# Kernel tuning notes

Hardware: AMD Instinct MI355X
Metric: run time of the kernel (lower is better)

Reference implementation:

```python
import jax, jax.numpy as jnp
import numpy as np

N = 100000   # nodes
E = 1600000  # edges
IN = 128     # input_dim
H = 64       # hidden_dim
OUT = 2      # output_dim
G = 64       # number of graphs in the batch


def setup_inputs() -> dict:
    key = jax.random.key(0)
    ks = jax.random.split(key, 12)
    x = jax.random.normal(ks[0], (N, IN), dtype=jnp.float32)
    edge_index = jax.random.randint(ks[1], (2, E), 0, N, dtype=jnp.int64)
    batch = jnp.sort(jax.random.randint(ks[2], (N,), 0, G, dtype=jnp.int64))
    s = 0.05
    return {
        "x": x,
        "edge_index": edge_index,
        "batch": batch,
        "W1": jax.random.normal(ks[3], (IN, H), dtype=jnp.float32) * s,
        "b1": jnp.zeros((H,), dtype=jnp.float32),
        "W2": jax.random.normal(ks[4], (H, H), dtype=jnp.float32) * s,
        "b2": jnp.zeros((H,), dtype=jnp.float32),
        "W3": jax.random.normal(ks[5], (H, H), dtype=jnp.float32) * s,
        "b3": jnp.zeros((H,), dtype=jnp.float32),
        "Wm1": jax.random.normal(ks[6], (H, H), dtype=jnp.float32) * s,
        "bm1": jnp.zeros((H,), dtype=jnp.float32),
        "Wm2": jax.random.normal(ks[7], (H, OUT), dtype=jnpp.float32) * s if False else jax.random.normal(ks[7], (H, OUT), dtype=jnp.float32) * s,
        "bm2": jnp.zeros((OUT,), dtype=jnp.float32),
    }


def _gcn_conv(x, W, b, src, dst, norm, n_nodes):
    # PyG GCNConv: h = x @ W; message = norm * h[src]; scatter-add at dst; + bias
    h = x @ W                                  # [N, H]
    msg = h[src] * norm[:, None]               # [E+N, H] gather + scale
    out = jax.ops.segment_sum(msg, dst, num_segments=n_nodes)
    return out + b


def reference(x, edge_index, batch, W1, b1, W2, b2, W3, b3, Wm1, bm1, Wm2, bm2):
    n = x.shape[0]
    # add self-loops (PyG GCNConv default add_self_loops=True)
    loop = jnp.arange(n, dtype=edge_index.dtype)
    src = jnp.concatenate([edge_index[0], loop])
    dst = jnp.concatenate([edge_index[1], loop])
    # symmetric normalization deg^-1/2 (deg over target nodes, incl. self-loops)
    deg = jax.ops.segment_sum(jnp.ones_like(dst, dtype=x.dtype), dst, num_segments=n)
    dinv = jnp.where(deg > 0, jax.lax.rsqrt(deg), 0.0)
    norm = dinv[src] * dinv[dst]               # [E+N]

    h = jax.nn.relu(_gcn_conv(x, W1, b1, src, dst, norm, n))   # dropout: eval -> identity
    h = jax.nn.relu(_gcn_conv(h, W2, b2, src, dst, norm, n))
    h = jax.nn.relu(_gcn_conv(h, W3, b3, src, dst, norm, n))

    # global_mean_pool over batch ids
    sums = jax.ops.segment_sum(h, batch, num_segments=G)       # [G, H]
    cnts = jax.ops.segment_sum(jnp.ones((n,), dtype=h.dtype), batch, num_segments=G)
    pooled = sums / jnp.maximum(cnts, 1.0)[:, None]

    # MLP head: Linear -> ReLU -> (Dropout eval) -> Linear
    z = jax.nn.relu(pooled @ Wm1 + bm1)
    return z @ Wm2 + bm2                                       # [G, OUT]
```

## Files before the change

### kernel.cpp

```cpp
#include <hip/hip_runtime.h>
#include <hip/hip_bf16.h>

#define NNODES 100000
#define NEDGES 1600000
#define IND 128
#define HD 64
#define OUTD 2
#define NG 64
#define BINSHIFT 9
#define BINSZ 512
#define BSTRIDE 12288
#define PB 256

typedef __attribute__((ext_vector_type(8))) short short8v;
typedef __attribute__((ext_vector_type(4))) float floatx4;

static __device__ __forceinline__ unsigned short f2bf(float f) {
    __hip_bfloat16 h = __float2bfloat16(f);
    return *(unsigned short*)&h;
}
static __device__ __forceinline__ float bf2f(unsigned short u) {
    __hip_bfloat16 h = *(__hip_bfloat16*)&u;
    return __bfloat162float(h);
}

__global__ __launch_bounds__(1024) void binP_kernel(const int* __restrict__ src,
                                                    const int* __restrict__ dst,
                                                    int* __restrict__ binCount,
                                                    unsigned int* __restrict__ binned,
                                                    int E, int nbins,
                                                    const float* __restrict__ W1,
                                                    const float* __restrict__ W2,
                                                    const float* __restrict__ W3,
                                                    unsigned short* __restrict__ WT1,
                                                    unsigned short* __restrict__ WT2,
                                                    unsigned short* __restrict__ WT3,
                                                    const int* __restrict__ batch,
                                                    float* __restrict__ gcnt, int n) {
    int blk = blockIdx.x;
    int t = threadIdx.x;
    if (blk >= PB) {
        int pb = blk - PB;
        if (pb == 0) {
            for (int i = t; i < 64 * IND + 64 * HD + 64 * HD; i += 1024) {
                if (i < 64 * IND) {
                    int nn2 = i / IND, k = i - nn2 * IND;
                    WT1[i] = f2bf(W1[k * 64 + nn2]);
                } else if (i < 64 * IND + 64 * HD) {
                    int j = i - 64 * IND;
                    int nn2 = j / HD, k = j - nn2 * HD;
                    WT2[j] = f2bf(W2[k * 64 + nn2]);
                } else {
                    int j = i - 64 * IND - 64 * HD;
                    int nn2 = j / HD, k = j - nn2 * HD;
                    WT3[j] = f2bf(W3[k * 64 + nn2]);
                }
            }
        } else {
            __shared__ float lg[NG];
            if (t < NG) lg[t] = 0.f;
            __syncthreads();
            const int nb2 = 19;
            int per = (n + nb2 - 1) / nb2;
            int i0 = (pb - 1) * per;
            int i1 = min(i0 + per, n);
            for (int i = i0 + t; i < i1; i += 1024)
                atomicAdd(&lg[batch[i]], 1.f);
            __syncthreads();
            if (t < NG) atomicAdd(&gcnt[t], lg[t]);
        }
        return;
    }
    __shared__ int lh[256];
    __shared__ int lbase[256];
    if (t < 256) lh[t] = 0;
    __syncthreads();
    int ebpb = (E + PB - 1) / PB;
    int e0 = blk * ebpb;
    int e1 = min(e0 + ebpb, E);
    int dcache[8];
    int ec = 0;
    for (int e = e0 + t; e < e1; e += 1024) {
        int d = dst[e];
        dcache[ec++] = d;
        atomicAdd(&lh[d >> BINSHIFT], 1);
    }
    __syncthreads();
    if (t < nbins) {
        int c = lh[t];
        if (c > 0) lbase[t] = atomicAdd(&binCount[t], c);
        lh[t] = 0;
    }
    __syncthreads();
    ec = 0;
    for (int e = e0 + t; e < e1; e += 1024) {
        int d = dcache[ec++];
        int b = d >> BINSHIFT;
        int idx = atomicAdd(&lh[b], 1);
        binned[(size_t)b * BSTRIDE + lbase[b] + idx] =
            ((unsigned int)(d & (BINSZ - 1)) << 17) | (unsigned int)src[e];
    }
}

__global__ __launch_bounds__(1024) void binHD_kernel(const unsigned int* __restrict__ binned,
                                                     const int* __restrict__ binCount,
                                                     float* __restrict__ dinv,
                                                     unsigned int* __restrict__ rowinfo,
                                                     int* __restrict__ ssrc, int n) {
    __shared__ int dh[BINSZ];
    __shared__ int rp[BINSZ];
    __shared__ int wsum[4];
    __shared__ unsigned int ecl[BSTRIDE];
    int b = blockIdx.x, t = threadIdx.x;
    int lane = t & 63, wv = t >> 6;
    if (t < BINSZ) dh[t] = 0;
    int s0 = b * BSTRIDE;
    int cnt = binCount[b];
    for (int i = t; i < cnt; i += 1024) ecl[i] = binned[s0 + i];
    __syncthreads();
    for (int i = t; i < cnt; i += 1024)
        atomicAdd(&dh[ecl[i] >> 17], 1);
    __syncthreads();
    if (t < BINSZ) {
        int node = (b << BINSHIFT) + t;
        if (node < n) dinv[node] = 1.0f / sqrtf((float)(dh[t] + 1));
    }
    int d0 = 0, d1 = 0, p = 0;
    if (t < 256) {
        d0 = (dh[2 * t] + 3) & ~3;
        d1 = (dh[2 * t + 1] + 3) & ~3;
        p = d0 + d1;
    }
    int sc = p;
#pragma unroll
    for (int d = 1; d < 64; d <<= 1) { int v = __shfl_up(sc, d, 64); if (lane >= d) sc += v; }
    if (t < 256 && lane == 63) wsum[wv] = sc;
    __syncthreads();
    if (t < 256) {
        int add = 0;
        for (int w2 = 0; w2 < wv; w2++) add += wsum[w2];
        int ex = sc - p + add;
        rp[2 * t]     = ex;
        rp[2 * t + 1] = ex + d0;
    }
    __syncthreads();
    if (t < BINSZ) {
        int node = (b << BINSHIFT) + t;
        if (node < n)
            rowinfo[node] = ((unsigned int)(s0 + rp[t]) << 10) |
                            (unsigned int)min(dh[t], 1023);
    }
    __syncthreads();
    for (int i = t; i < cnt; i += 1024) {
        unsigned int rec = ecl[i];
        int doff = rec >> 17;
        int s = rec & 0x1FFFF;
        int idx = atomicSub(&dh[doff], 1) - 1;
        ssrc[s0 + rp[doff] + idx] = s;
    }
}

template <int K, bool BF16IN>
__global__ __launch_bounds__(256) void mm_mfma_kernel(const void* __restrict__ Xv,
                                                      const unsigned short* __restrict__ WT,
                                                      const float* __restrict__ dinv,
                                                      unsigned short* __restrict__ Tb, int nn) {
    const int lane = threadIdx.x & 63;
    const int wv   = threadIdx.x >> 6;
    const int nb   = blockIdx.x * 64 + wv * 16;
    if (nb >= nn) return;
    const int col  = lane & 15;
    const int quad = lane >> 4;
    const int m    = min(nb + col, nn - 1);

    floatx4 acc0 = {0.f, 0.f, 0.f, 0.f};
    floatx4 acc1 = {0.f, 0.f, 0.f, 0.f};
    floatx4 acc2 = {0.f, 0.f, 0.f, 0.f};
    floatx4 acc3 = {0.f, 0.f, 0.f, 0.f};

#pragma unroll
    for (int ks = 0; ks < K; ks += 32) {
        const int k0 = ks + quad * 8;
        short8v a;
        if (BF16IN) {
            a = *(const short8v*)((const unsigned short*)Xv + (size_t)m * K + k0);
        } else {
            const float* xr = (const float*)Xv + (size_t)m * K + k0;
            float4 f0 = *(const float4*)(xr);
            float4 f1 = *(const float4*)(xr + 4);
            a[0] = (short)f2bf(f0.x); a[1] = (short)f2bf(f0.y);
            a[2] = (short)f2bf(f0.z); a[3] = (short)f2bf(f0.w);
            a[4] = (short)f2bf(f1.x); a[5] = (short)f2bf(f1.y);
            a[6] = (short)f2bf(f1.z); a[7] = (short)f2bf(f1.w);
        }
        short8v b0 = *(const short8v*)(WT + (size_t)(4 * col + 0) * K + k0);
        short8v b1 = *(const short8v*)(WT + (size_t)(4 * col + 1) * K + k0);
        short8v b2 = *(const short8v*)(WT + (size_t)(4 * col + 2) * K + k0);
        short8v b3 = *(const short8v*)(WT + (size_t)(4 * col + 3) * K + k0);
        acc0 = __builtin_amdgcn_mfma_f32_16x16x32_bf16(a, b0, acc0, 0, 0, 0);
        acc1 = __builtin_amdgcn_mfma_f32_16x16x32_bf16(a, b1, acc1, 0, 0, 0);
        acc2 = __builtin_amdgcn_mfma_f32_16x16x32_bf16(a, b2, acc2, 0, 0, 0);
        acc3 = __builtin_amdgcn_mfma_f32_16x16x32_bf16(a, b3, acc3, 0, 0, 0);
    }

#pragma unroll
    for (int r = 0; r < 4; r++) {
        int node = nb + quad * 4 + r;
        if (node < nn) {
            float sc = dinv[node];
            unsigned int lo = (unsigned int)f2bf(sc * acc0[r]) |
                              ((unsigned int)f2bf(sc * acc1[r]) << 16);
            unsigned int hi = (unsigned int)f2bf(sc * acc2[r]) |
                              ((unsigned int)f2bf(sc * acc3[r]) << 16);
            uint2 st; st.x = lo; st.y = hi;
            ((uint2*)Tb)[(size_t)node * 16 + col] = st;
        }
    }
}

__global__ __launch_bounds__(256) void agg_kernel(const unsigned short* __restrict__ Tb,
                                                  const unsigned int* __restrict__ rowinfo,
                                                  const int* __restrict__ ssrc,
                                                  const float* __restrict__ dinv,
                                                  const float* __restrict__ bias,
                                                  unsigned short* __restrict__ Ob, int nn) {
    int wave = __builtin_amdgcn_readfirstlane((blockIdx.x * 256 + threadIdx.x) >> 6);
    int lane = threadIdx.x & 63;
    if (wave >= nn) return;
    int n = wave;
    float acc = bf2f(Tb[(size_t)n * 64 + lane]);
    unsigned int info = rowinfo[n];
    int rb = (int)(info >> 10);
    int re = rb + (int)(info & 1023);
    int i = rb;
    for (; i + 16 <= re; i += 16) {
        int s[16];
#pragma unroll
        for (int k = 0; k < 16; k++) s[k] = ssrc[i + k];
        float v[16];
#pragma unroll
        for (int k = 0; k < 16; k++) v[k] = bf2f(Tb[(size_t)s[k] * 64 + lane]);
#pragma unroll
        for (int k = 0; k < 16; k++) acc += v[k];
    }
    for (; i + 4 <= re; i += 4) {
        int s0 = ssrc[i], s1 = ssrc[i + 1], s2 = ssrc[i + 2], s3 = ssrc[i + 3];
        float v0 = bf2f(Tb[(size_t)s0 * 64 + lane]);
        float v1 = bf2f(Tb[(size_t)s1 * 64 + lane]);
        float v2 = bf2f(Tb[(size_t)s2 * 64 + lane]);
        float v3 = bf2f(Tb[(size_t)s3 * 64 + lane]);
        acc += v0; acc += v1; acc += v2; acc += v3;
    }
    for (; i < re; i++)
        acc += bf2f(Tb[(size_t)ssrc[i] * 64 + lane]);
    float o = dinv[n] * acc + bias[lane];
    o = o > 0.f ? o : 0.f;
    Ob[(size_t)n * 64 + lane] = f2bf(o);
}

__global__ __launch_bounds__(256) void pool_kernel(const unsigned short* __restrict__ Hb,
                                                   const int* __restrict__ batch,
                                                   float* __restrict__ pooled, int nn) {
    int wid = (blockIdx.x * 256 + threadIdx.x) >> 6;
    int lane = threadIdx.x & 63;
    int nwaves = (gridDim.x * 256) >> 6;
    int per = (nn + nwaves - 1) / nwaves;
    int n0 = wid * per;
    int n1 = n0 + per; if (n1 > nn) n1 = nn;
    if (n0 >= n1) return;
    int cur = batch[n0];
    float acc = 0.f;
    for (int n = n0; n < n1; ++n) {
        int g = batch[n];
        if (g != cur) {
            atomicAdd(&pooled[cur * 64 + lane], acc);
            acc = 0.f; cur = g;
        }
        acc += bf2f(Hb[(size_t)n * 64 + lane]);
    }
    atomicAdd(&pooled[cur * 64 + lane], acc);
}

__global__ __launch_bounds__(256) void head_kernel(const float* __restrict__ pooled,
                                                   const float* __restrict__ gcnt,
                                                   const float* __restrict__ Wm1,
                                                   const float* __restrict__ bm1,
                                                   const float* __restrict__ Wm2,
                                                   const float* __restrict__ bm2,
                                                   float* __restrict__ out) {
    __shared__ float P[NG * 64];
    __shared__ float Z[NG * 64];
    int tid = threadIdx.x;
    for (int i = tid; i < NG * 64; i += 256) {
        int g = i >> 6;
        float c = gcnt[g];
        c = c > 1.f ? c : 1.f;
        P[i] = pooled[i] / c;
    }
    __syncthreads();
    for (int i = tid; i < NG * 64; i += 256) {
        int g = i >> 6, j = i & 63;
        float a = bm1[j];
#pragma unroll 8
        for (int k = 0; k < 64; ++k) a += P[g * 64 + k] * Wm1[k * 64 + j];
        Z[i] = a > 0.f ? a : 0.f;
    }
    __syncthreads();
    for (int i = tid; i < NG * OUTD; i += 256) {
        int g = i / OUTD, o = i % OUTD;
        float a = bm2[o];
#pragma unroll 8
        for (int k = 0; k < 64; ++k) a += Z[g * 64 + k] * Wm2[k * OUTD + o];
        out[i] = a;
    }
}

extern "C" void kernel_launch(void* const* d_in, const int* in_sizes, int n_in,
                              void* d_out, int out_size, void* d_ws, size_t ws_size,
                              hipStream_t stream) {
    const float* x    = (const float*)d_in[0];
    const int*  edge  = (const int*)d_in[1];
    const int*  batch = (const int*)d_in[2];
    const float* W1 = (const float*)d_in[3];
    const float* b1 = (const float*)d_in[4];
    const float* W2 = (const float*)d_in[5];
    const float* b2 = (const float*)d_in[6];
    const float* W3 = (const float*)d_in[7];
    const float* b3 = (const float*)d_in[8];
    const float* Wm1 = (const float*)d_in[9];
    const float* bm1 = (const float*)d_in[10];
    const float* Wm2 = (const float*)d_in[11];
    const float* bm2 = (const float*)d_in[12];

    const int N_ = in_sizes[2];
    const int E_ = in_sizes[1] / 2;
    const int* src = edge;
    const int* dst = edge + E_;
    const int nbins = (N_ + BINSZ - 1) >> BINSHIFT;

    char* w = (char*)d_ws;
    auto alloc = [&](size_t bytes) -> void* {
        void* p = (void*)w;
        w += (bytes + 255) & ~(size_t)255;
        return p;
    };
    float* dinv   = (float*)alloc((size_t)N_ * 4);
    unsigned int* rowinfo = (unsigned int*)alloc((size_t)N_ * 4);
    float* pooled = (float*)alloc((size_t)(NG * 64 + NG) * 4);
    int*   binCount = (int*)alloc(256 * 4);
    float* gcnt   = pooled + NG * 64;
    int*   ssrc   = (int*)alloc((size_t)nbins * BSTRIDE * 4);
    unsigned int* binned = (unsigned int*)alloc((size_t)nbins * BSTRIDE * 4);
    unsigned short* Tb  = (unsigned short*)alloc((size_t)N_ * 64 * 2);
    unsigned short* hBb = (unsigned short*)alloc((size_t)N_ * 64 * 2);
    unsigned short* WT1 = (unsigned short*)alloc((size_t)64 * IND * 2);
    unsigned short* WT2 = (unsigned short*)alloc((size_t)64 * HD * 2);
    unsigned short* WT3 = (unsigned short*)alloc((size_t)64 * HD * 2);

    hipMemsetAsync(pooled, 0, (size_t)(NG * 64 + NG) * 4 + 256 * 4 + 256, stream);

    binP_kernel<<<PB + 20, 1024, 0, stream>>>(src, dst, binCount, binned, E_, nbins,
                                              W1, W2, W3, WT1, WT2, WT3, batch, gcnt, N_);
    binHD_kernel<<<nbins, 1024, 0, stream>>>(binned, binCount, dinv, rowinfo, ssrc, N_);

    const int mmblk = (N_ + 63) / 64;
    const int aggblk = (N_ + 3) / 4;

    mm_mfma_kernel<IND, false><<<mmblk, 256, 0, stream>>>(x, WT1, dinv, Tb, N_);
    agg_kernel<<<aggblk, 256, 0, stream>>>(Tb, rowinfo, ssrc, dinv, b1, hBb, N_);
    mm_mfma_kernel<HD, true><<<mmblk, 256, 0, stream>>>(hBb, WT2, dinv, Tb, N_);
    agg_kernel<<<aggblk, 256, 0, stream>>>(Tb, rowinfo, ssrc, dinv, b2, hBb, N_);
    mm_mfma_kernel<HD, true><<<mmblk, 256, 0, stream>>>(hBb, WT3, dinv, Tb, N_);
    agg_kernel<<<aggblk, 256, 0, stream>>>(Tb, rowinfo, ssrc, dinv, b3, hBb, N_);

    pool_kernel<<<256, 256, 0, stream>>>(hBb, batch, pooled, N_);
    head_kernel<<<1, 256, 0, stream>>>(pooled, gcnt, Wm1, bm1, Wm2, bm2, (float*)d_out);
}
```

Measured before the change: 370.7 us.

## Fuse layer-2/3 dense transforms into aggregation epilogue and derive graph counts from sorted batch

Removes the separate MFMA matmul kernels for layers 2 and 3. Instead, each aggregation wave stages its ReLU'd row in LDS and multiplies it by the next layer's fp32 weight matrix, loaded into LDS per block, then writes the dinv-prescaled result directly. It also drops the WT2/WT3 bf16 transposes and the per-graph count pass, computing graph sizes in the head kernel by binary search over the sorted batch array. The goal is to save two kernel launches and the write and read of intermediate node features. In exchange, every 4-node block reloads a 16KB weight tile and does the matvec in fp32 FMA on LDS rather than on matrix cores.

Result: slower. 387.5 us (+4.5%).

```diff
diff --git a/kernel.cpp b/kernel.cpp
--- a/kernel.cpp
+++ b/kernel.cpp
@@ -30,44 +30,13 @@
                                                     unsigned int* __restrict__ binned,
                                                     int E, int nbins,
                                                     const float* __restrict__ W1,
-                                                    const float* __restrict__ W2,
-                                                    const float* __restrict__ W3,
-                                                    unsigned short* __restrict__ WT1,
-                                                    unsigned short* __restrict__ WT2,
-                                                    unsigned short* __restrict__ WT3,
-                                                    const int* __restrict__ batch,
-                                                    float* __restrict__ gcnt, int n) {
+                                                    unsigned short* __restrict__ WT1) {
     int blk = blockIdx.x;
     int t = threadIdx.x;
     if (blk >= PB) {
-        int pb = blk - PB;
-        if (pb == 0) {
-            for (int i = t; i < 64 * IND + 64 * HD + 64 * HD; i += 1024) {
-                if (i < 64 * IND) {
-                    int nn2 = i / IND, k = i - nn2 * IND;
-                    WT1[i] = f2bf(W1[k * 64 + nn2]);
-                } else if (i < 64 * IND + 64 * HD) {
-                    int j = i - 64 * IND;
-                    int nn2 = j / HD, k = j - nn2 * HD;
-                    WT2[j] = f2bf(W2[k * 64 + nn2]);
-                } else {
-                    int j = i - 64 * IND - 64 * HD;
-                    int nn2 = j / HD, k = j - nn2 * HD;
-                    WT3[j] = f2bf(W3[k * 64 + nn2]);
-                }
-            }
-        } else {
-            __shared__ float lg[NG];
-            if (t < NG) lg[t] = 0.f;
-            __syncthreads();
-            const int nb2 = 19;
-            int per = (n + nb2 - 1) / nb2;
-            int i0 = (pb - 1) * per;
-            int i1 = min(i0 + per, n);
-            for (int i = i0 + t; i < i1; i += 1024)
-                atomicAdd(&lg[batch[i]], 1.f);
-            __syncthreads();
-            if (t < NG) atomicAdd(&gcnt[t], lg[t]);
+        for (int i = t; i < 64 * IND; i += 1024) {
+            int nn2 = i / IND, k = i - nn2 * IND;
+            WT1[i] = f2bf(W1[k * 64 + nn2]);
         }
         return;
     }
@@ -160,8 +129,7 @@
     }
 }
 
-template <int K, bool BF16IN>
-__global__ __launch_bounds__(256) void mm_mfma_kernel(const void* __restrict__ Xv,
+__global__ __launch_bounds__(256) void mm_mfma_kernel(const float* __restrict__ Xv,
                                                       const unsigned short* __restrict__ WT,
                                                       const float* __restrict__ dinv,
                                                       unsigned short* __restrict__ Tb, int nn) {
@@ -179,24 +147,20 @@
     floatx4 acc3 = {0.f, 0.f, 0.f, 0.f};
 
 #pragma unroll
-    for (int ks = 0; ks < K; ks += 32) {
+    for (int ks = 0; ks < IND; ks += 32) {
         const int k0 = ks + quad * 8;
+        const float* xr = Xv + (size_t)m * IND + k0;
+        float4 f0 = *(const float4*)(xr);
+        float4 f1 = *(const float4*)(xr + 4);
         short8v a;
-        if (BF16IN) {
-            a = *(const short8v*)((const unsigned short*)Xv + (size_t)m * K + k0);
-        } else {
-            const float* xr = (const float*)Xv + (size_t)m * K + k0;
-            float4 f0 = *(const float4*)(xr);
-            float4 f1 = *(const float4*)(xr + 4);
-            a[0] = (short)f2bf(f0.x); a[1] = (short)f2bf(f0.y);
-            a[2] = (short)f2bf(f0.z); a[3] = (short)f2bf(f0.w);
-            a[4] = (short)f2bf(f1.x); a[5] = (short)f2bf(f1.y);
-            a[6] = (short)f2bf(f1.z); a[7] = (short)f2bf(f1.w);
-        }
-        short8v b0 = *(const short8v*)(WT + (size_t)(4 * col + 0) * K + k0);
-        short8v b1 = *(const short8v*)(WT + (size_t)(4 * col + 1) * K + k0);
-        short8v b2 = *(const short8v*)(WT + (size_t)(4 * col + 2) * K + k0);
-        short8v b3 = *(const short8v*)(WT + (size_t)(4 * col + 3) * K + k0);
+        a[0] = (short)f2bf(f0.x); a[1] = (short)f2bf(f0.y);
+        a[2] = (short)f2bf(f0.z); a[3] = (short)f2bf(f0.w);
+        a[4] = (short)f2bf(f1.x); a[5] = (short)f2bf(f1.y);
+        a[6] = (short)f2bf(f1.z); a[7] = (short)f2bf(f1.w);
+        short8v b0 = *(const short8v*)(WT + (size_t)(4 * col + 0) * IND + k0);
+        short8v b1 = *(const short8v*)(WT + (size_t)(4 * col + 1) * IND + k0);
+        short8v b2 = *(const short8v*)(WT + (size_t)(4 * col + 2) * IND + k0);
+        short8v b3 = *(const short8v*)(WT + (size_t)(4 * col + 3) * IND + k0);
         acc0 = __builtin_amdgcn_mfma_f32_16x16x32_bf16(a, b0, acc0, 0, 0, 0);
         acc1 = __builtin_amdgcn_mfma_f32_16x16x32_bf16(a, b1, acc1, 0, 0, 0);
         acc2 = __builtin_amdgcn_mfma_f32_16x16x32_bf16(a, b2, acc2, 0, 0, 0);
@@ -218,16 +182,29 @@
     }
 }
 
+template <int FUSE>
 __global__ __launch_bounds__(256) void agg_kernel(const unsigned short* __restrict__ Tb,
                                                   const unsigned int* __restrict__ rowinfo,
                                                   const int* __restrict__ ssrc,
                                                   const float* __restrict__ dinv,
                                                   const float* __restrict__ bias,
+                                                  const float* __restrict__ W,
                                                   unsigned short* __restrict__ Ob, int nn) {
+    __shared__ float WL[FUSE ? 64 * 64 : 1];
+    __shared__ float rowbuf[FUSE ? 4 * 64 : 1];
+    if (FUSE) {
+        const float4* Wv = (const float4*)W;
+#pragma unroll
+        for (int i = 0; i < 4; i++)
+            ((float4*)WL)[threadIdx.x + 256 * i] = Wv[threadIdx.x + 256 * i];
+        __syncthreads();
+    }
     int wave = __builtin_amdgcn_readfirstlane((blockIdx.x * 256 + threadIdx.x) >> 6);
     int lane = threadIdx.x & 63;
+    int wv = (threadIdx.x >> 6);
     if (wave >= nn) return;
     int n = wave;
+    float dn = dinv[n];
     float acc = bf2f(Tb[(size_t)n * 64 + lane]);
     unsigned int info = rowinfo[n];
     int rb = (int)(info >> 10);
@@ -253,9 +230,18 @@
     }
     for (; i < re; i++)
         acc += bf2f(Tb[(size_t)ssrc[i] * 64 + lane]);
-    float o = dinv[n] * acc + bias[lane];
+    float o = dn * acc + bias[lane];
     o = o > 0.f ? o : 0.f;
-    Ob[(size_t)n * 64 + lane] = f2bf(o);
+    if (FUSE) {
+        rowbuf[wv * 64 + lane] = o;
+        float t = 0.f;
+#pragma unroll 16
+        for (int k = 0; k < 64; ++k)
+            t += rowbuf[wv * 64 + k] * WL[k * 64 + lane];
+        Ob[(size_t)n * 64 + lane] = f2bf(dn * t);
+    } else {
+        Ob[(size_t)n * 64 + lane] = f2bf(o);
+    }
 }
 
 __global__ __launch_bounds__(256) void pool_kernel(const unsigned short* __restrict__ Hb,
@@ -281,19 +267,28 @@
     atomicAdd(&pooled[cur * 64 + lane], acc);
 }
 
+static __device__ __forceinline__ int lbound(const int* __restrict__ a, int n, int key) {
+    int lo = 0, hi = n;
+    while (lo < hi) { int mid = (lo + hi) >> 1; if (a[mid] < key) lo = mid + 1; else hi = mid; }
+    return lo;
+}
+
 __global__ __launch_bounds__(256) void head_kernel(const float* __restrict__ pooled,
-                                                   const float* __restrict__ gcnt,
+                                                   const int* __restrict__ batch,
                                                    const float* __restrict__ Wm1,
                                                    const float* __restrict__ bm1,
                                                    const float* __restrict__ Wm2,
                                                    const float* __restrict__ bm2,
-                                                   float* __restrict__ out) {
+                                                   float* __restrict__ out, int nn) {
     __shared__ float P[NG * 64];
     __shared__ float Z[NG * 64];
+    __shared__ int bnds[NG + 1];
     int tid = threadIdx.x;
+    if (tid <= NG) bnds[tid] = (tid == 0) ? 0 : ((tid == NG) ? nn : lbound(batch, nn, tid));
+    __syncthreads();
     for (int i = tid; i < NG * 64; i += 256) {
         int g = i >> 6;
-        float c = gcnt[g];
+        float c = (float)(bnds[g + 1] - bnds[g]);
         c = c > 1.f ? c : 1.f;
         P[i] = pooled[i] / c;
     }
@@ -344,35 +339,31 @@
         w += (bytes + 255) & ~(size_t)255;
         return p;
     };
+    int*   binCount = (int*)alloc(256 * 4);
+    float* pooled   = (float*)alloc((size_t)NG * 64 * 4);
     float* dinv   = (float*)alloc((size_t)N_ * 4);
     unsigned int* rowinfo = (unsigned int*)alloc((size_t)N_ * 4);
-    float* pooled = (float*)alloc((size_t)(NG * 64 + NG) * 4);
-    int*   binCount = (int*)alloc(256 * 4);
-    float* gcnt   = pooled + NG * 64;
     int*   ssrc   = (int*)alloc((size_t)nbins * BSTRIDE * 4);
     unsigned int* binned = (unsigned int*)alloc((size_t)nbins * BSTRIDE * 4);
     unsigned short* Tb  = (unsigned short*)alloc((size_t)N_ * 64 * 2);
     unsigned short* hBb = (unsigned short*)alloc((size_t)N_ * 64 * 2);
     unsigned short* WT1 = (unsigned short*)alloc((size_t)64 * IND * 2);
-    unsigned short* WT2 = (unsigned short*)alloc((size_t)64 * HD * 2);
-    unsigned short* WT3 = (unsigned short*)alloc((size_t)64 * HD * 2);
-
-    hipMemsetAsync(pooled, 0, (size_t)(NG * 64 + NG) * 4 + 256 * 4 + 256, stream);
-
-    binP_kernel<<<PB + 20, 1024, 0, stream>>>(src, dst, binCount, binned, E_, nbins,
-                                              W1, W2, W3, WT1, WT2, WT3, batch, gcnt, N_);
+
+    hipMemsetAsync(binCount, 0, 256 * 4 + (size_t)NG * 64 * 4, stream);
+
+    binP_kernel<<<PB + 1, 1024, 0, stream>>>(src, dst, binCount, binned, E_, nbins,
+                                             W1, WT1);
     binHD_kernel<<<nbins, 1024, 0, stream>>>(binned, binCount, dinv, rowinfo, ssrc, N_);
 
     const int mmblk = (N_ + 63) / 64;
     const int aggblk = (N_ + 3) / 4;
 
-    mm_mfma_kernel<IND, false><<<mmblk, 256, 0, stream>>>(x, WT1, dinv, Tb, N_);
-    agg_kernel<<<aggblk, 256, 0, stream>>>(Tb, rowinfo, ssrc, dinv, b1, hBb, N_);
-    mm_mfma_kernel<HD, true><<<mmblk, 256, 0, stream>>>(hBb, WT2, dinv, Tb, N_);
-    agg_kernel<<<aggblk, 256, 0, stream>>>(Tb, rowinfo, ssrc, dinv, b2, hBb, N_);
-    mm_mfma_kernel<HD, true><<<mmblk, 256, 0, stream>>>(hBb, WT3, dinv, Tb, N_);
-    agg_kernel<<<aggblk, 256, 0, stream>>>(Tb, rowinfo, ssrc, dinv, b3, hBb, N_);
+    mm_mfma_kernel<<<mmblk, 256, 0, stream>>>(x, WT1, dinv, Tb, N_);
+    agg_kernel<1><<<aggblk, 256, 0, stream>>>(Tb, rowinfo, ssrc, dinv, b1, W2, hBb, N_);
+    agg_kernel<1><<<aggblk, 256, 0, stream>>>(hBb, rowinfo, ssrc, dinv, b2, W3, Tb, N_);
+    agg_kernel<0><<<aggblk, 256, 0, stream>>>(Tb, rowinfo, ssrc, dinv, b3, nullptr, hBb, N_);
 
     pool_kernel<<<256, 256, 0, stream>>>(hBb, batch, pooled, N_);
-    head_kernel<<<1, 256, 0, stream>>>(pooled, gcnt, Wm1, bm1, Wm2, bm2, (float*)d_out);
-}
+    head_kernel<<<1, 256, 0, stream>>>(pooled, batch, Wm1, bm1, Wm2, bm2,
+                                       (float*)d_out, N_);
+}
```
